# Kernel optimization log

Hardware: AMD Instinct MI355X
Metric: run time of the kernel (lower is better)

## Reference

```python
import jax, jax.numpy as jnp
import numpy as np

D, H, L, FF, IN, OUT, S, B = 512, 8, 6, 2048, 32, 3, 512, 32


def setup_inputs() -> dict:
    key = jax.random.key(0)
    ks = iter(jax.random.split(key, 32))
    w = lambda shape: jax.random.normal(next(ks), shape, jnp.float32) * 0.02
    z = lambda shape: jnp.zeros(shape, jnp.float32)
    o = lambda shape: jnp.ones(shape, jnp.float32)
    return {
        'x': jax.random.normal(next(ks), (B, S, IN), jnp.float32),
        'w_in': w((IN, D)), 'b_in': z((D,)), 'g_in': o((D,)), 'be_in': z((D,)),
        'w_qkv': w((L, D, 3 * D)), 'b_qkv': z((L, 3 * D)),
        'w_out': w((L, D, D)), 'b_out': z((L, D)),
        'g1': o((L, D)), 'be1': z((L, D)),
        'w_ff1': w((L, D, FF)), 'b_ff1': z((L, FF)),
        'w_ff2': w((L, FF, D)), 'b_ff2': z((L, D)),
        'g2': o((L, D)), 'be2': z((L, D)),
        'w_h1': w((D, D // 2)), 'b_h1': z((D // 2,)),
        'w_h2': w((D // 2, OUT)), 'b_h2': z((OUT,)),
    }


def _layer_norm(x, g, b, eps=1e-5):
    mu = jnp.mean(x, axis=-1, keepdims=True)
    var = jnp.mean(jnp.square(x - mu), axis=-1, keepdims=True)
    return (x - mu) / jnp.sqrt(var + eps) * g + b


def _gelu(x):
    return jax.nn.gelu(x, approximate=False)  # torch nn.GELU default (erf)


def _pos_encoding(seq_len, d_model):
    pos = jnp.arange(seq_len, dtype=jnp.float32)[:, None]
    div = jnp.exp(jnp.arange(0, d_model, 2, dtype=jnp.float32) * (-np.log(10000.0) / d_model))
    pe = jnp.zeros((seq_len, d_model), jnp.float32)
    pe = pe.at[:, 0::2].set(jnp.sin(pos * div))
    pe = pe.at[:, 1::2].set(jnp.cos(pos * div))
    return pe


def reference(x, w_in, b_in, g_in, be_in, w_qkv, b_qkv, w_out, b_out,
              g1, be1, w_ff1, b_ff1, w_ff2, b_ff2, g2, be2,
              w_h1, b_h1, w_h2, b_h2):
    b, s, _ = x.shape
    d = w_in.shape[1]
    hd = d // H
    scale = hd ** -0.5

    # input projection: Linear -> LayerNorm -> GELU (dropout = identity at eval)
    h = _gelu(_layer_norm(x @ w_in + b_in, g_in, be_in))
    h = h + _pos_encoding(s, d)

    causal_mask = jnp.triu(jnp.ones((s, s), bool), 1)  # True above diagonal = future

    for l in range(w_qkv.shape[0]):
        qkv = (h @ w_qkv[l] + b_qkv[l]).reshape(b, s, 3, H, hd)
        q, k, v = qkv[:, :, 0], qkv[:, :, 1], qkv[:, :, 2]  # [b, s, H, hd]
        scores = jnp.einsum('bihd,bjhd->bhij', q, k) * scale
        scores = jnp.where(causal_mask, -jnp.inf, scores)
        attn = jax.nn.softmax(scores, axis=-1)
        o = jnp.einsum('bhij,bjhd->bihd', attn, v).reshape(b, s, d)
        o = o @ w_out[l] + b_out[l]
        h = _layer_norm(h + o, g1[l], be1[l])
        f = _gelu(h @ w_ff1[l] + b_ff1[l]) @ w_ff2[l] + b_ff2[l]
        h = _layer_norm(h + f, g2[l], be2[l])

    logits = _gelu(h @ w_h1 + b_h1) @ w_h2 + b_h2  # [b, s, OUT]
    return logits[:, -1, :]  # last position only
```

## Files before the change

kernel.cpp:

```cpp
#include <hip/hip_runtime.h>
#include <hip/hip_bf16.h>
#include <math.h>

#define D_   512
#define H_   8
#define HD_  64
#define L_   6
#define FF_  2048
#define IN_  32
#define OUT_ 3
#define S_   512
#define B_   32
#define M_   (B_ * S_)

typedef __attribute__((ext_vector_type(8))) short short8;
typedef __attribute__((ext_vector_type(4))) float floatx4;

__device__ __forceinline__ float gelu_f(float x) {
    return 0.5f * x * (1.0f + erff(x * 0.7071067811865475f));
}
__device__ __forceinline__ float bf2f(unsigned short u) {
    union { unsigned int i; float f; } c; c.i = ((unsigned)u) << 16; return c.f;
}
__device__ __forceinline__ unsigned short f2bf(float v) {
    __hip_bfloat16 t = __float2bfloat16(v);
    return *(unsigned short*)&t;
}
__device__ __forceinline__ void async16(const void* g, void* l) {
    __builtin_amdgcn_global_load_lds(
        (const __attribute__((address_space(1))) unsigned int*)g,
        (__attribute__((address_space(3))) unsigned int*)l, 16, 0, 0);
}

template<int DO_GELU, int OUT_BF16, int ADD_RES, int PIPE>
__global__ __launch_bounds__(256)
void gemm_mfma_k(const __hip_bfloat16* __restrict__ A,
                 const __hip_bfloat16* __restrict__ WT,
                 const float* __restrict__ bias,
                 const float* __restrict__ R,
                 void* __restrict__ C,
                 int N, int K) {
    __shared__ __align__(16) char smem[PIPE ? 65536 : 34816];
    float* Ep = (float*)smem;

    const int tid  = threadIdx.x;
    const int lane = tid & 63;
    const int wave = tid >> 6;

    const int Lid = blockIdx.y * gridDim.x + blockIdx.x;
    const int xcd = Lid & 7;
    const int idx = Lid >> 3;
    const int gx  = gridDim.x, gy8 = gridDim.y >> 3;
    const int m0 = (xcd * gy8 + idx / gx) * 128;
    const int n0 = (idx % gx) * 128;

    const int wm = (wave >> 1) * 64, wn = (wave & 1) * 64;

    const int srow = tid >> 2;
    const int scol = ((tid & 3) ^ (srow & 3)) * 8;
    const short* Ag = (const short*)A + (long)(m0 + srow) * K + scol;
    const short* Bg = (const short*)WT + (long)(n0 + srow) * K + scol;

    floatx4 acc[4][4];
    #pragma unroll
    for (int i = 0; i < 4; i++)
        #pragma unroll
        for (int j = 0; j < 4; j++) acc[i][j] = (floatx4)0.f;

    const int r = lane & 15, q = lane >> 4;
    const int qa = (q ^ (r & 3)) * 8;

    if (PIPE) {
        const int nIter = K >> 6;
        {
            short* As_ = (short*)smem;
            short* Bs_ = (short*)(smem + 16384);
            async16(Ag,                     As_ + tid * 8);
            async16(Ag + (long)64 * K,      As_ + 2048 + tid * 8);
            async16(Ag + 32,                As_ + 4096 + tid * 8);
            async16(Ag + (long)64 * K + 32, As_ + 6144 + tid * 8);
            async16(Bg,                     Bs_ + tid * 8);
            async16(Bg + (long)64 * K,      Bs_ + 2048 + tid * 8);
            async16(Bg + 32,                Bs_ + 4096 + tid * 8);
            async16(Bg + (long)64 * K + 32, Bs_ + 6144 + tid * 8);
        }
        for (int i = 0; i < nIter; i++) {
            __syncthreads();
            if (i + 1 < nIter) {
                const int k0 = (i + 1) << 6;
                short* As_ = (short*)(smem + ((i + 1) & 1) * 32768);
                short* Bs_ = (short*)(smem + ((i + 1) & 1) * 32768 + 16384);
                async16(Ag + k0,                     As_ + tid * 8);
                async16(Ag + (long)64 * K + k0,      As_ + 2048 + tid * 8);
                async16(Ag + k0 + 32,                As_ + 4096 + tid * 8);
                async16(Ag + (long)64 * K + k0 + 32, As_ + 6144 + tid * 8);
                async16(Bg + k0,                     Bs_ + tid * 8);
                async16(Bg + (long)64 * K + k0,      Bs_ + 2048 + tid * 8);
                async16(Bg + k0 + 32,                Bs_ + 4096 + tid * 8);
                async16(Bg + (long)64 * K + k0 + 32, Bs_ + 6144 + tid * 8);
            }
            const short* As_ = (const short*)(smem + (i & 1) * 32768);
            const short* Bs_ = (const short*)(smem + (i & 1) * 32768 + 16384);
            #pragma unroll
            for (int c = 0; c < 2; c++) {
                const short* Asc = As_ + c * 4096;
                const short* Bsc = Bs_ + c * 4096;
                short8 af[4], bf[4];
                #pragma unroll
                for (int t = 0; t < 4; t++)
                    af[t] = *(const short8*)&Asc[(wm + t * 16 + r) * 32 + qa];
                #pragma unroll
                for (int t = 0; t < 4; t++)
                    bf[t] = *(const short8*)&Bsc[(wn + t * 16 + r) * 32 + qa];
                #pragma unroll
                for (int i2 = 0; i2 < 4; i2++)
                    #pragma unroll
                    for (int j = 0; j < 4; j++)
                        acc[i2][j] = __builtin_amdgcn_mfma_f32_16x16x32_bf16(
                            af[i2], bf[j], acc[i2][j], 0, 0, 0);
            }
        }
        __syncthreads();
    } else {
        short* As0 = (short*)(smem);
        short* As1 = (short*)(smem + 8192);
        short* Bs0 = (short*)(smem + 16384);
        short* Bs1 = (short*)(smem + 24576);
        for (int k0 = 0; k0 < K; k0 += 64) {
            async16(Ag + k0,                     As0 + tid * 8);
            async16(Ag + (long)64 * K + k0,      As0 + 2048 + tid * 8);
            async16(Ag + k0 + 32,                As1 + tid * 8);
            async16(Ag + (long)64 * K + k0 + 32, As1 + 2048 + tid * 8);
            async16(Bg + k0,                     Bs0 + tid * 8);
            async16(Bg + (long)64 * K + k0,      Bs0 + 2048 + tid * 8);
            async16(Bg + k0 + 32,                Bs1 + tid * 8);
            async16(Bg + (long)64 * K + k0 + 32, Bs1 + 2048 + tid * 8);
            __syncthreads();
            #pragma unroll
            for (int c = 0; c < 2; c++) {
                const short* Asc = c ? As1 : As0;
                const short* Bsc = c ? Bs1 : Bs0;
                short8 af[4], bf[4];
                #pragma unroll
                for (int t = 0; t < 4; t++)
                    af[t] = *(const short8*)&Asc[(wm + t * 16 + r) * 32 + qa];
                #pragma unroll
                for (int t = 0; t < 4; t++)
                    bf[t] = *(const short8*)&Bsc[(wn + t * 16 + r) * 32 + qa];
                #pragma unroll
                for (int i = 0; i < 4; i++)
                    #pragma unroll
                    for (int j = 0; j < 4; j++)
                        acc[i][j] = __builtin_amdgcn_mfma_f32_16x16x32_bf16(
                            af[i], bf[j], acc[i][j], 0, 0, 0);
            }
            __syncthreads();
        }
    }

    const int erow = tid >> 5;
    const int ecol = (tid & 31) * 4;
    const float4 bvec = *(const float4*)&bias[n0 + ecol];

    #pragma unroll
    for (int pass = 0; pass < 2; pass++) {
        if (pass) __syncthreads();
        if ((wave >> 1) == pass) {
            #pragma unroll
            for (int i = 0; i < 4; i++)
                #pragma unroll
                for (int j = 0; j < 4; j++)
                    #pragma unroll
                    for (int rg = 0; rg < 4; rg++)
                        Ep[(i * 16 + q * 4 + rg) * 132 + wn + j * 16 + r] =
                            acc[i][j][rg];
        }
        __syncthreads();
        #pragma unroll
        for (int it = 0; it < 8; it++) {
            const int row = it * 8 + erow;
            const long grow = (long)(m0 + pass * 64 + row) * N + n0 + ecol;
            const float4 v = *(const float4*)&Ep[row * 132 + ecol];
            float o0 = v.x + bvec.x, o1 = v.y + bvec.y;
            float o2 = v.z + bvec.z, o3 = v.w + bvec.w;
            if (DO_GELU) {
                o0 = gelu_f(o0); o1 = gelu_f(o1);
                o2 = gelu_f(o2); o3 = gelu_f(o3);
            }
            if (ADD_RES) {
                const float4 rv = *(const float4*)&R[grow];
                o0 += rv.x; o1 += rv.y; o2 += rv.z; o3 += rv.w;
            }
            if (OUT_BF16) {
                ushort4 pk;
                pk.x = f2bf(o0); pk.y = f2bf(o1);
                pk.z = f2bf(o2); pk.w = f2bf(o3);
                *(ushort4*)((unsigned short*)C + grow) = pk;
            } else {
                *(float4*)((float*)C + grow) = make_float4(o0, o1, o2, o3);
            }
        }
    }
}

__global__ __launch_bounds__(256)
void transpose_cast_k(const float* __restrict__ W, __hip_bfloat16* __restrict__ WT,
                      int K, int N) {
    __shared__ float tile[32][33];
    const float* Wl = W + (long)blockIdx.z * K * N;
    __hip_bfloat16* WTl = WT + (long)blockIdx.z * K * N;
    const int n0 = blockIdx.x * 32, k0 = blockIdx.y * 32;
    const int tx = threadIdx.x & 31, ty = threadIdx.x >> 5;
    for (int rr = ty; rr < 32; rr += 8)
        tile[rr][tx] = Wl[(long)(k0 + rr) * N + n0 + tx];
    __syncthreads();
    for (int rr = ty; rr < 32; rr += 8)
        WTl[(long)(n0 + rr) * K + k0 + tx] = __float2bfloat16(tile[tx][rr]);
}

template<int DO_GELU>
__global__ __launch_bounds__(256)
void gemm_bias_k(const float* __restrict__ A, long lda,
                 const float* __restrict__ W,
                 const float* __restrict__ bias,
                 float* __restrict__ C,
                 int M, int N, int K) {
    __shared__ float As[16][64];
    __shared__ float Ws[16][64];
    const int tx = threadIdx.x;
    const int ty = threadIdx.y;
    const int tid = ty * 16 + tx;
    const int m0 = blockIdx.y * 64;
    const int n0 = blockIdx.x * 64;
    float acc[4][4] = {};
    for (int k0 = 0; k0 < K; k0 += 16) {
        #pragma unroll
        for (int e = tid; e < 64 * 16; e += 256) {
            int m = e >> 4, k = e & 15;
            float v = 0.f;
            if (m0 + m < M) v = A[(long)(m0 + m) * lda + k0 + k];
            As[k][m] = v;
        }
        #pragma unroll
        for (int e = tid; e < 16 * 64; e += 256) {
            int k = e >> 6, n = e & 63;
            float v = 0.f;
            if (n0 + n < N) v = W[(long)(k0 + k) * N + n0 + n];
            Ws[k][n] = v;
        }
        __syncthreads();
        #pragma unroll
        for (int kk = 0; kk < 16; kk++) {
            float a[4], w[4];
            #pragma unroll
            for (int i = 0; i < 4; i++) a[i] = As[kk][ty * 4 + i];
            #pragma unroll
            for (int j = 0; j < 4; j++) w[j] = Ws[kk][tx * 4 + j];
            #pragma unroll
            for (int i = 0; i < 4; i++)
                #pragma unroll
                for (int j = 0; j < 4; j++)
                    acc[i][j] += a[i] * w[j];
        }
        __syncthreads();
    }
    #pragma unroll
    for (int i = 0; i < 4; i++) {
        int m = m0 + ty * 4 + i;
        if (m >= M) continue;
        #pragma unroll
        for (int j = 0; j < 4; j++) {
            int n = n0 + tx * 4 + j;
            if (n >= N) continue;
            float v = acc[i][j] + bias[n];
            if (DO_GELU) v = gelu_f(v);
            C[(long)m * N + n] = v;
        }
    }
}

__global__ __launch_bounds__(256)
void ln_k(const float* __restrict__ X,
          const float* __restrict__ g,
          const float* __restrict__ be,
          float* __restrict__ H,
          __hip_bfloat16* __restrict__ Hb) {
    const int row = blockIdx.x * 4 + (threadIdx.x >> 6);
    const int lane = threadIdx.x & 63;
    const float* xp = X + (long)row * D_ + lane * 8;
    const float4 a = *(const float4*)xp;
    const float4 c = *(const float4*)(xp + 4);
    float s = a.x + a.y + a.z + a.w + c.x + c.y + c.z + c.w;
    #pragma unroll
    for (int off = 1; off < 64; off <<= 1) s += __shfl_xor(s, off);
    const float mu = s * (1.0f / D_);
    float d[8] = { a.x - mu, a.y - mu, a.z - mu, a.w - mu,
                   c.x - mu, c.y - mu, c.z - mu, c.w - mu };
    float ss = 0.f;
    #pragma unroll
    for (int e = 0; e < 8; e++) ss += d[e] * d[e];
    #pragma unroll
    for (int off = 1; off < 64; off <<= 1) ss += __shfl_xor(ss, off);
    const float inv = 1.0f / sqrtf(ss * (1.0f / D_) + 1e-5f);
    const float4 g0 = *(const float4*)(g + lane * 8);
    const float4 g1 = *(const float4*)(g + lane * 8 + 4);
    const float4 e0 = *(const float4*)(be + lane * 8);
    const float4 e1 = *(const float4*)(be + lane * 8 + 4);
    const float gv[8] = { g0.x, g0.y, g0.z, g0.w, g1.x, g1.y, g1.z, g1.w };
    const float ev[8] = { e0.x, e0.y, e0.z, e0.w, e1.x, e1.y, e1.z, e1.w };
    float o[8];
    short8 pk;
    #pragma unroll
    for (int e = 0; e < 8; e++) {
        o[e] = d[e] * inv * gv[e] + ev[e];
        pk[e] = (short)f2bf(o[e]);
    }
    float* hp = H + (long)row * D_ + lane * 8;
    *(float4*)hp = make_float4(o[0], o[1], o[2], o[3]);
    *(float4*)(hp + 4) = make_float4(o[4], o[5], o[6], o[7]);
    *(short8*)((unsigned short*)Hb + (long)row * D_ + lane * 8) = pk;
}

__global__ __launch_bounds__(256)
void ln_gelu_pos_k(const float* __restrict__ X,
                   const float* __restrict__ g,
                   const float* __restrict__ be,
                   float* __restrict__ Hout,
                   __hip_bfloat16* __restrict__ Hb) {
    const int row = blockIdx.x;
    const int s = row & (S_ - 1);
    const int t = threadIdx.x;
    const float* x = X + (long)row * D_;
    float v0 = x[t], v1 = x[t + 256];
    __shared__ float red[256];
    red[t] = v0 + v1;
    __syncthreads();
    for (int off = 128; off; off >>= 1) {
        if (t < off) red[t] += red[t + off];
        __syncthreads();
    }
    float mu = red[0] * (1.0f / D_);
    __syncthreads();
    float d0 = v0 - mu, d1 = v1 - mu;
    red[t] = d0 * d0 + d1 * d1;
    __syncthreads();
    for (int off = 128; off; off >>= 1) {
        if (t < off) red[t] += red[t + off];
        __syncthreads();
    }
    float var = red[0] * (1.0f / D_);
    float inv = 1.0f / sqrtf(var + 1e-5f);
    float o0 = gelu_f(d0 * inv * g[t] + be[t]);
    float o1 = gelu_f(d1 * inv * g[t + 256] + be[t + 256]);
    {
        int d = t, i = d >> 1;
        float dv = expf((float)(2 * i) * (-9.210340371976184f / 512.0f));
        float ang = (float)s * dv;
        o0 += (d & 1) ? cosf(ang) : sinf(ang);
    }
    {
        int d = t + 256, i = d >> 1;
        float dv = expf((float)(2 * i) * (-9.210340371976184f / 512.0f));
        float ang = (float)s * dv;
        o1 += (d & 1) ? cosf(ang) : sinf(ang);
    }
    Hout[(long)row * D_ + t] = o0;
    Hout[(long)row * D_ + t + 256] = o1;
    Hb[(long)row * D_ + t] = __float2bfloat16(o0);
    Hb[(long)row * D_ + t + 256] = __float2bfloat16(o1);
}

#define LDT 72
__global__ __launch_bounds__(256)
void attn_mfma_k(const __hip_bfloat16* __restrict__ qkv,
                 __hip_bfloat16* __restrict__ O) {
    const int qt = blockIdx.x;
    const int bh = blockIdx.y;
    const int b = bh >> 3, h = bh & (H_ - 1);
    const int tid = threadIdx.x;
    const int wave = tid >> 6, lane = tid & 63;
    const int ln = lane & 15, quad = lane >> 4;
    const int wm = wave * 32;
    const int i0 = qt * 128;

    __shared__ unsigned short Qs[128 * LDT];
    __shared__ unsigned short Ks[64 * LDT];
    __shared__ unsigned short Vt[64 * LDT];
    __shared__ unsigned short Ps[128 * LDT];
    __shared__ float stat[128];

    const unsigned short* base = (const unsigned short*)qkv + (long)b * S_ * (3 * D_);

    {
        const int r0 = tid >> 3, c0 = (tid & 7) * 8;
        #pragma unroll
        for (int i = 0; i < 4; i++) {
            const int rw = i * 32 + r0;
            *(short8*)&Qs[rw * LDT + c0] =
                *(const short8*)(base + (long)(i0 + rw) * (3 * D_) + h * HD_ + c0);
        }
    }

    float m_i[2] = { -INFINITY, -INFINITY };
    float l_i[2] = { 0.f, 0.f };
    floatx4 o_acc[2][4];
    #pragma unroll
    for (int i = 0; i < 2; i++)
        #pragma unroll
        for (int j = 0; j < 4; j++) o_acc[i][j] = (floatx4)0.f;

    const int kr = tid >> 2, kc = (tid & 3) * 16;
    const int vj = tid & 63, vc = (tid >> 6) * 16;

    const int ktmax = 2 * qt + 1;
    for (int kt = 0; kt <= ktmax; kt++) {
        const int j0 = kt * 64;
        {
            const unsigned short* kp = base + (long)(j0 + kr) * (3 * D_) + D_ + h * HD_ + kc;
            *(short8*)&Ks[kr * LDT + kc]     = *(const short8*)(kp);
            *(short8*)&Ks[kr * LDT + kc + 8] = *(const short8*)(kp + 8);
            const unsigned short* vp = base + (long)(j0 + vj) * (3 * D_) + 2 * D_ + h * HD_ + vc;
            short8 v0 = *(const short8*)(vp);
            short8 v1 = *(const short8*)(vp + 8);
            #pragma unroll
            for (int e = 0; e < 8; e++) {
                Vt[(vc + e) * LDT + vj]     = (unsigned short)v0[e];
                Vt[(vc + 8 + e) * LDT + vj] = (unsigned short)v1[e];
            }
        }
        __syncthreads();

        floatx4 sa[4][2];
        #pragma unroll
        for (int mt = 0; mt < 4; mt++)
            #pragma unroll
            for (int nt = 0; nt < 2; nt++) sa[mt][nt] = (floatx4)0.f;
        #pragma unroll
        for (int c = 0; c < 2; c++) {
            short8 kf[4], qf[2];
            #pragma unroll
            for (int mt = 0; mt < 4; mt++)
                kf[mt] = *(const short8*)&Ks[(mt * 16 + ln) * LDT + c * 32 + quad * 8];
            #pragma unroll
            for (int nt = 0; nt < 2; nt++)
                qf[nt] = *(const short8*)&Qs[(wm + nt * 16 + ln) * LDT + c * 32 + quad * 8];
            #pragma unroll
            for (int mt = 0; mt < 4; mt++)
                #pragma unroll
                for (int nt = 0; nt < 2; nt++)
                    sa[mt][nt] = __builtin_amdgcn_mfma_f32_16x16x32_bf16(
                        kf[mt], qf[nt], sa[mt][nt], 0, 0, 0);
        }

        const bool domask = (kt >= 2 * qt);
        #pragma unroll
        for (int nt = 0; nt < 2; nt++) {
            const int qg = i0 + wm + nt * 16 + ln;
            float mx = -INFINITY;
            #pragma unroll
            for (int mt = 0; mt < 4; mt++)
                #pragma unroll
                for (int rg = 0; rg < 4; rg++) {
                    float v = sa[mt][nt][rg] * 0.125f;
                    if (domask && (j0 + mt * 16 + quad * 4 + rg > qg)) v = -INFINITY;
                    sa[mt][nt][rg] = v;
                    mx = fmaxf(mx, v);
                }
            mx = fmaxf(mx, __shfl_xor(mx, 16));
            mx = fmaxf(mx, __shfl_xor(mx, 32));
            const float mn = fmaxf(m_i[nt], mx);
            const float alpha = __expf(m_i[nt] - mn);
            m_i[nt] = mn;
            float ls = 0.f;
            #pragma unroll
            for (int mt = 0; mt < 4; mt++) {
                ushort4 pk;
                float p0 = __expf(sa[mt][nt][0] - mn);
                float p1 = __expf(sa[mt][nt][1] - mn);
                float p2 = __expf(sa[mt][nt][2] - mn);
                float p3 = __expf(sa[mt][nt][3] - mn);
                ls += p0 + p1 + p2 + p3;
                pk.x = f2bf(p0); pk.y = f2bf(p1); pk.z = f2bf(p2); pk.w = f2bf(p3);
                *(ushort4*)&Ps[(wm + nt * 16 + ln) * LDT + mt * 16 + quad * 4] = pk;
            }
            ls += __shfl_xor(ls, 16);
            ls += __shfl_xor(ls, 32);
            l_i[nt] = l_i[nt] * alpha + ls;
            if (quad == 0) stat[wm + nt * 16 + ln] = alpha;
        }

        #pragma unroll
        for (int mt2 = 0; mt2 < 2; mt2++) {
            #pragma unroll
            for (int rg = 0; rg < 4; rg++) {
                const float a = stat[wm + mt2 * 16 + quad * 4 + rg];
                #pragma unroll
                for (int nt = 0; nt < 4; nt++) o_acc[mt2][nt][rg] *= a;
            }
        }

        #pragma unroll
        for (int c = 0; c < 2; c++) {
            short8 pf[2], vf[4];
            #pragma unroll
            for (int mt2 = 0; mt2 < 2; mt2++)
                pf[mt2] = *(const short8*)&Ps[(wm + mt2 * 16 + ln) * LDT + c * 32 + quad * 8];
            #pragma unroll
            for (int nt = 0; nt < 4; nt++)
                vf[nt] = *(const short8*)&Vt[(nt * 16 + ln) * LDT + c * 32 + quad * 8];
            #pragma unroll
            for (int mt2 = 0; mt2 < 2; mt2++)
                #pragma unroll
                for (int nt = 0; nt < 4; nt++)
                    o_acc[mt2][nt] = __builtin_amdgcn_mfma_f32_16x16x32_bf16(
                        pf[mt2], vf[nt], o_acc[mt2][nt], 0, 0, 0);
        }
        __syncthreads();
    }

    if (quad == 0) {
        stat[wm + ln]      = l_i[0];
        stat[wm + 16 + ln] = l_i[1];
    }
    unsigned short* Og = (unsigned short*)O;
    #pragma unroll
    for (int mt2 = 0; mt2 < 2; mt2++) {
        #pragma unroll
        for (int rg = 0; rg < 4; rg++) {
            const float linv = 1.0f / stat[wm + mt2 * 16 + quad * 4 + rg];
            const long row = (long)(b * S_ + i0 + wm + mt2 * 16 + quad * 4 + rg);
            #pragma unroll
            for (int nt = 0; nt < 4; nt++)
                Og[row * D_ + h * HD_ + nt * 16 + ln] =
                    f2bf(o_acc[mt2][nt][rg] * linv);
        }
    }
}

__global__ __launch_bounds__(256)
void head1_k(const float* __restrict__ h, const float* __restrict__ w1,
             const float* __restrict__ b1, float* __restrict__ th) {
    __shared__ float hs[D_];
    const int b = blockIdx.x, n = threadIdx.x;
    const float* hr = h + (long)(b * S_ + S_ - 1) * D_;
    hs[n] = hr[n];
    hs[n + 256] = hr[n + 256];
    __syncthreads();
    float s = 0.f;
    #pragma unroll 8
    for (int k = 0; k < D_; k++) s += hs[k] * w1[(long)k * 256 + n];
    th[b * 256 + n] = gelu_f(s + b1[n]);
}

__global__ __launch_bounds__(64)
void head2_k(const float* __restrict__ th, const float* __restrict__ w2,
             const float* __restrict__ b2, float* __restrict__ out) {
    const int b = blockIdx.x, lane = threadIdx.x;
    const float* t = th + b * 256;
    float s0 = 0.f, s1 = 0.f, s2 = 0.f;
    #pragma unroll
    for (int e = 0; e < 4; e++) {
        const int k = lane * 4 + e;
        const float tv = t[k];
        s0 += tv * w2[k * 3 + 0];
        s1 += tv * w2[k * 3 + 1];
        s2 += tv * w2[k * 3 + 2];
    }
    #pragma unroll
    for (int off = 1; off < 64; off <<= 1) {
        s0 += __shfl_xor(s0, off);
        s1 += __shfl_xor(s1, off);
        s2 += __shfl_xor(s2, off);
    }
    if (lane == 0) {
        out[b * 3 + 0] = s0 + b2[0];
        out[b * 3 + 1] = s1 + b2[1];
        out[b * 3 + 2] = s2 + b2[2];
    }
}

extern "C" void kernel_launch(void* const* d_in, const int* in_sizes, int n_in,
                              void* d_out, int out_size, void* d_ws, size_t ws_size,
                              hipStream_t stream) {
    const float* x     = (const float*)d_in[0];
    const float* w_in  = (const float*)d_in[1];
    const float* b_in  = (const float*)d_in[2];
    const float* g_in  = (const float*)d_in[3];
    const float* be_in = (const float*)d_in[4];
    const float* w_qkv = (const float*)d_in[5];
    const float* b_qkv = (const float*)d_in[6];
    const float* w_out = (const float*)d_in[7];
    const float* b_out = (const float*)d_in[8];
    const float* g1    = (const float*)d_in[9];
    const float* be1   = (const float*)d_in[10];
    const float* w_ff1 = (const float*)d_in[11];
    const float* b_ff1 = (const float*)d_in[12];
    const float* w_ff2 = (const float*)d_in[13];
    const float* b_ff2 = (const float*)d_in[14];
    const float* g2    = (const float*)d_in[15];
    const float* be2   = (const float*)d_in[16];
    const float* w_h1  = (const float*)d_in[17];
    const float* b_h1  = (const float*)d_in[18];
    const float* w_h2  = (const float*)d_in[19];
    const float* b_h2  = (const float*)d_in[20];
    float* out = (float*)d_out;

    float* h    = (float*)d_ws;
    float* bufB = h + (long)M_ * D_;
    float* th   = bufB + (long)M_ * D_;
    __hip_bfloat16* hb    = (__hip_bfloat16*)(th + 32 * 256);
    __hip_bfloat16* attb  = hb + (long)M_ * D_;
    __hip_bfloat16* bufAb = attb + (long)M_ * D_;
    __hip_bfloat16* qkvT  = bufAb + (long)M_ * FF_;
    __hip_bfloat16* outT  = qkvT + (long)L_ * (3 * D_) * D_;
    __hip_bfloat16* ff1T  = outT + (long)L_ * D_ * D_;
    __hip_bfloat16* ff2T  = ff1T + (long)L_ * FF_ * D_;

    dim3 blk(16, 16);

    transpose_cast_k<<<dim3((3 * D_) / 32, D_ / 32, L_), 256, 0, stream>>>(w_qkv, qkvT, D_, 3 * D_);
    transpose_cast_k<<<dim3(D_ / 32, D_ / 32, L_), 256, 0, stream>>>(w_out, outT, D_, D_);
    transpose_cast_k<<<dim3(FF_ / 32, D_ / 32, L_), 256, 0, stream>>>(w_ff1, ff1T, D_, FF_);
    transpose_cast_k<<<dim3(D_ / 32, FF_ / 32, L_), 256, 0, stream>>>(w_ff2, ff2T, FF_, D_);

    gemm_bias_k<0><<<dim3(D_ / 64, M_ / 64), blk, 0, stream>>>(
        x, IN_, w_in, b_in, bufB, M_, D_, IN_);
    ln_gelu_pos_k<<<M_, 256, 0, stream>>>(bufB, g_in, be_in, h, hb);

    for (int l = 0; l < L_; l++) {
        gemm_mfma_k<0, 1, 0, 1><<<dim3((3 * D_) / 128, M_ / 128), 256, 0, stream>>>(
            hb, qkvT + (long)l * (3 * D_) * D_, b_qkv + l * 3 * D_, nullptr,
            bufAb, 3 * D_, D_);
        attn_mfma_k<<<dim3(S_ / 128, B_ * H_), 256, 0, stream>>>(bufAb, attb);
        gemm_mfma_k<0, 0, 1, 1><<<dim3(D_ / 128, M_ / 128), 256, 0, stream>>>(
            attb, outT + (long)l * D_ * D_, b_out + l * D_, h,
            bufB, D_, D_);
        ln_k<<<M_ / 4, 256, 0, stream>>>(bufB, g1 + l * D_, be1 + l * D_, h, hb);
        gemm_mfma_k<1, 1, 0, 0><<<dim3(FF_ / 128, M_ / 128), 256, 0, stream>>>(
            hb, ff1T + (long)l * FF_ * D_, b_ff1 + l * FF_, nullptr,
            bufAb, FF_, D_);
        gemm_mfma_k<0, 0, 1, 1><<<dim3(D_ / 128, M_ / 128), 256, 0, stream>>>(
            bufAb, ff2T + (long)l * D_ * FF_, b_ff2 + l * D_, h,
            bufB, D_, FF_);
        ln_k<<<M_ / 4, 256, 0, stream>>>(bufB, g2 + l * D_, be2 + l * D_, h, hb);
    }

    head1_k<<<B_, 256, 0, stream>>>(h, w_h1, b_h1, th);
    head2_k<<<B_, 64, 0, stream>>>(th, w_h2, b_h2, out);
}
```

Baseline: 1.645 ms.

## Add 256x256-tile 512-thread MFMA GEMM for QKV and FF1, faster erf GELU

Adds a new GEMM kernel with 256x256 output tiles, 8 waves, a double-buffered 128KB LDS pipeline using async global-to-LDS loads, explicit barriers and priority hints. It is used for the QKV and FF1 projections, which are the wider-N GEMMs. The goal is more data reuse per tile and less global traffic. It also replaces erff in GELU with an Abramowitz-Stegun polynomial using a hardware reciprocal and fast exp, trading a little accuracy for cheaper epilogue math. The large LDS footprint limits occupancy, and the QKV grid (6x64 blocks) may underfill the GPU.

```diff
diff --git a/kernel.cpp b/kernel.cpp
--- a/kernel.cpp
+++ b/kernel.cpp
@@ -17,7 +17,16 @@
 typedef __attribute__((ext_vector_type(4))) float floatx4;
 
 __device__ __forceinline__ float gelu_f(float x) {
-    return 0.5f * x * (1.0f + erff(x * 0.7071067811865475f));
+    const float ax = fabsf(x) * 0.70710678118654752f;
+    const float t = __builtin_amdgcn_rcpf(fmaf(0.3275911f, ax, 1.0f));
+    float p = fmaf(1.061405429f, t, -1.453152027f);
+    p = fmaf(p, t, 1.421413741f);
+    p = fmaf(p, t, -0.284496736f);
+    p = fmaf(p, t, 0.254829592f);
+    p = p * t;
+    const float e = __expf(-ax * ax);
+    const float er = copysignf(fmaf(-p, e, 1.0f), x);
+    return 0.5f * x * (1.0f + er);
 }
 __device__ __forceinline__ float bf2f(unsigned short u) {
     union { unsigned int i; float f; } c; c.i = ((unsigned)u) << 16; return c.f;
@@ -30,6 +39,170 @@
     __builtin_amdgcn_global_load_lds(
         (const __attribute__((address_space(1))) unsigned int*)g,
         (__attribute__((address_space(3))) unsigned int*)l, 16, 0, 0);
+}
+__device__ __forceinline__ void stage2(const short* g, char* d, long rs) {
+    async16(g, d);
+    async16(g + rs, d + 8192);
+}
+
+#define MFMA_ROW(ai, accr)                                                    \
+    accr[0] = __builtin_amdgcn_mfma_f32_16x16x32_bf16(ai, b[0], accr[0], 0, 0, 0); \
+    accr[1] = __builtin_amdgcn_mfma_f32_16x16x32_bf16(ai, b[1], accr[1], 0, 0, 0); \
+    accr[2] = __builtin_amdgcn_mfma_f32_16x16x32_bf16(ai, b[2], accr[2], 0, 0, 0); \
+    accr[3] = __builtin_amdgcn_mfma_f32_16x16x32_bf16(ai, b[3], accr[3], 0, 0, 0);
+
+#define MFMA_PHASE(B0)                                                        \
+    __builtin_amdgcn_s_barrier();                                             \
+    asm volatile("s_waitcnt lgkmcnt(0)" ::: "memory");                        \
+    __builtin_amdgcn_sched_barrier(0);                                        \
+    __builtin_amdgcn_s_setprio(1);                                            \
+    MFMA_ROW(a[0], acc[B0 + 0])                                               \
+    MFMA_ROW(a[1], acc[B0 + 1])                                               \
+    MFMA_ROW(a[2], acc[B0 + 2])                                               \
+    MFMA_ROW(a[3], acc[B0 + 3])                                               \
+    __builtin_amdgcn_s_setprio(0);
+
+template<int DO_GELU, int OUT_BF16, int ADD_RES>
+__global__ __launch_bounds__(512, 2)
+void gemm_mfma256_k(const __hip_bfloat16* __restrict__ A,
+                    const __hip_bfloat16* __restrict__ WT,
+                    const float* __restrict__ bias,
+                    const float* __restrict__ R,
+                    void* __restrict__ C,
+                    int N, int K) {
+    __shared__ __align__(16) char smem[131072];
+
+    const int tid  = threadIdx.x;
+    const int lane = tid & 63;
+    const int wave = tid >> 6;
+
+    const int Lid = blockIdx.y * gridDim.x + blockIdx.x;
+    const int xcd = Lid & 7;
+    const int idx = Lid >> 3;
+    const int gx  = gridDim.x, gy8 = gridDim.y >> 3;
+    const int m0 = (xcd * gy8 + idx / gx) * 256;
+    const int n0 = (idx % gx) * 256;
+
+    const int wm = (wave >> 2) * 128;
+    const int wn = (wave & 3) * 64;
+    const int r = lane & 15, q = lane >> 4;
+    const int qa = (q ^ (r & 3)) * 8;
+
+    const int srow = tid >> 2;
+    const int sc = ((tid & 3) ^ (srow & 3)) * 8;
+    const short* Ag = (const short*)A + (long)(m0 + srow) * K + sc;
+    const short* Bg = (const short*)WT + (long)(n0 + srow) * K + sc;
+    const long rs = (long)128 * K;
+
+    floatx4 acc[8][4];
+    #pragma unroll
+    for (int i = 0; i < 8; i++)
+        #pragma unroll
+        for (int j = 0; j < 4; j++) acc[i][j] = (floatx4)0.f;
+
+    const int NT = K >> 6;
+
+    stage2(Ag,      smem         + tid * 16, rs);
+    stage2(Bg,      smem + 32768 + tid * 16, rs);
+    stage2(Ag + 32, smem + 16384 + tid * 16, rs);
+    stage2(Bg + 32, smem + 49152 + tid * 16, rs);
+    asm volatile("s_waitcnt vmcnt(4)" ::: "memory");
+    __builtin_amdgcn_s_barrier();
+
+    short8 a[4], b[4];
+    for (int t = 0; t < NT; ++t) {
+        const int cur = t & 1, nxt = cur ^ 1;
+        const bool hn = (t + 1 < NT);
+        const short* As = (const short*)(smem + cur * 65536);
+        const short* Bs = (const short*)(smem + cur * 65536 + 32768);
+        const short* Agt = Ag + (t + 1) * 64;
+        const short* Bgt = Bg + (t + 1) * 64;
+        char* Ad = smem + nxt * 65536;
+        char* Bd = smem + nxt * 65536 + 32768;
+
+        #pragma unroll
+        for (int i = 0; i < 4; i++)
+            a[i] = *(const short8*)&As[(wm + i * 16 + r) * 32 + qa];
+        #pragma unroll
+        for (int j = 0; j < 4; j++)
+            b[j] = *(const short8*)&Bs[(wn + j * 16 + r) * 32 + qa];
+        if (hn) stage2(Agt, Ad + tid * 16, rs);
+        MFMA_PHASE(0)
+        __builtin_amdgcn_s_barrier();
+
+        #pragma unroll
+        for (int i = 0; i < 4; i++)
+            a[i] = *(const short8*)&As[(wm + 64 + i * 16 + r) * 32 + qa];
+        if (hn) stage2(Bgt, Bd + tid * 16, rs);
+        MFMA_PHASE(4)
+        if (hn) asm volatile("s_waitcnt vmcnt(4)" ::: "memory");
+        else    asm volatile("s_waitcnt vmcnt(0)" ::: "memory");
+        __builtin_amdgcn_s_barrier();
+
+        #pragma unroll
+        for (int i = 0; i < 4; i++)
+            a[i] = *(const short8*)&As[8192 + (wm + i * 16 + r) * 32 + qa];
+        #pragma unroll
+        for (int j = 0; j < 4; j++)
+            b[j] = *(const short8*)&Bs[8192 + (wn + j * 16 + r) * 32 + qa];
+        if (hn) stage2(Agt + 32, Ad + 16384 + tid * 16, rs);
+        MFMA_PHASE(0)
+        __builtin_amdgcn_s_barrier();
+
+        #pragma unroll
+        for (int i = 0; i < 4; i++)
+            a[i] = *(const short8*)&As[8192 + (wm + 64 + i * 16 + r) * 32 + qa];
+        if (hn) stage2(Bgt + 32, Bd + 16384 + tid * 16, rs);
+        MFMA_PHASE(4)
+        if (hn) asm volatile("s_waitcnt vmcnt(4)" ::: "memory");
+        __builtin_amdgcn_s_barrier();
+    }
+
+    float* Ef = (float*)smem;
+    const int erow = tid >> 3;
+    const int ej = tid & 7;
+    #pragma unroll
+    for (int ch = 0; ch < 4; ch++) {
+        __builtin_amdgcn_s_barrier();
+        if ((wave >> 2) == (ch >> 1)) {
+            #pragma unroll
+            for (int mf2 = 0; mf2 < 4; mf2++) {
+                const int mf = (ch & 1) * 4 + mf2;
+                #pragma unroll
+                for (int nf = 0; nf < 4; nf++)
+                    #pragma unroll
+                    for (int rg = 0; rg < 4; rg++)
+                        Ef[(mf2 * 16 + q * 4 + rg) * 260 + wn + nf * 16 + r] =
+                            acc[mf][nf][rg];
+            }
+        }
+        __builtin_amdgcn_s_barrier();
+        #pragma unroll
+        for (int e = 0; e < 8; e++) {
+            const int c4 = ej + e * 8;
+            const long grow = (long)(m0 + ch * 64 + erow) * N + n0 + c4 * 4;
+            const float4 v = *(const float4*)&Ef[erow * 260 + c4 * 4];
+            const float4 bv = *(const float4*)&bias[n0 + c4 * 4];
+            float o0 = v.x + bv.x, o1 = v.y + bv.y;
+            float o2 = v.z + bv.z, o3 = v.w + bv.w;
+            if (DO_GELU) {
+                o0 = gelu_f(o0); o1 = gelu_f(o1);
+                o2 = gelu_f(o2); o3 = gelu_f(o3);
+            }
+            if (ADD_RES) {
+                const float4 rv = *(const float4*)&R[grow];
+                o0 += rv.x; o1 += rv.y; o2 += rv.z; o3 += rv.w;
+            }
+            if (OUT_BF16) {
+                ushort4 pk;
+                pk.x = f2bf(o0); pk.y = f2bf(o1);
+                pk.z = f2bf(o2); pk.w = f2bf(o3);
+                *(ushort4*)((unsigned short*)C + grow) = pk;
+            } else {
+                *(float4*)((float*)C + grow) = make_float4(o0, o1, o2, o3);
+            }
+        }
+    }
 }
 
 template<int DO_GELU, int OUT_BF16, int ADD_RES, int PIPE>
@@ -628,7 +801,7 @@
     ln_gelu_pos_k<<<M_, 256, 0, stream>>>(bufB, g_in, be_in, h, hb);
 
     for (int l = 0; l < L_; l++) {
-        gemm_mfma_k<0, 1, 0, 1><<<dim3((3 * D_) / 128, M_ / 128), 256, 0, stream>>>(
+        gemm_mfma256_k<0, 1, 0><<<dim3((3 * D_) / 256, M_ / 256), 512, 0, stream>>>(
             hb, qkvT + (long)l * (3 * D_) * D_, b_qkv + l * 3 * D_, nullptr,
             bufAb, 3 * D_, D_);
         attn_mfma_k<<<dim3(S_ / 128, B_ * H_), 256, 0, stream>>>(bufAb, attb);
@@ -636,7 +809,7 @@
             attb, outT + (long)l * D_ * D_, b_out + l * D_, h,
             bufB, D_, D_);
         ln_k<<<M_ / 4, 256, 0, stream>>>(bufB, g1 + l * D_, be1 + l * D_, h, hb);
-        gemm_mfma_k<1, 1, 0, 0><<<dim3(FF_ / 128, M_ / 128), 256, 0, stream>>>(
+        gemm_mfma256_k<1, 1, 0><<<dim3(FF_ / 256, M_ / 256), 512, 0, stream>>>(
             hb, ff1T + (long)l * FF_ * D_, b_ff1 + l * FF_, nullptr,
             bufAb, FF_, D_);
         gemm_mfma_k<0, 0, 1, 1><<<dim3(D_ / 128, M_ / 128), 256, 0, stream>>>(
```

Measured after the change: 1.669 ms. Within noise of the previous version (+1.5%).
